# Kernel optimization log

Measured on AMD Instinct MI355X. Metric: run time of the kernel, lower is better.

The kernel has to match this reference:

```python
import jax, jax.numpy as jnp
import numpy as np

G = 128        # number of graphs
N = 512        # nodes per graph
F_IN = 128     # n_feat
H = 128        # agg_hidden
L = 5          # n_layer
FC = 128       # fc_hidden
C = 10         # n_class
E_HALF = 8192  # undirected edge pairs per graph (symmetrized -> 16384 directed)


def setup_inputs() -> dict:
    key = jax.random.key(0)
    ks = jax.random.split(key, 8)
    x = jax.random.normal(ks[0], (G * N, F_IN), dtype=jnp.float32)
    # per-graph random edges, offset into the block-diagonal node index space
    s = jax.random.randint(ks[1], (G, E_HALF), 0, N)
    d = jax.random.randint(ks[2], (G, E_HALF), 0, N)
    off = (jnp.arange(G) * N)[:, None]
    s = (s + off).reshape(-1)
    d = (d + off).reshape(-1)
    src = jnp.concatenate([s, d])  # symmetric adjacency (edges + reversed)
    dst = jnp.concatenate([d, s])
    eps = jnp.zeros((L,), jnp.float32)  # nn.Parameter(torch.zeros(n_layer))
    W = jax.random.normal(ks[3], (L, H, H), jnp.float32) / jnp.sqrt(H)
    b = jnp.zeros((L, H), jnp.float32)
    fc1_w = jax.random.normal(ks[4], (H, FC), jnp.float32) / jnp.sqrt(H)
    fc1_b = jnp.zeros((FC,), jnp.float32)
    fc2_w = jax.random.normal(ks[5], (FC, C), jnp.float32) / jnp.sqrt(FC)
    fc2_b = jnp.zeros((C,), jnp.float32)
    return {"x": x, "eps": eps, "W": W, "b": b,
            "fc1_w": fc1_w, "fc1_b": fc1_b, "fc2_w": fc2_w, "fc2_b": fc2_b,
            "src": src, "dst": dst}


def reference(x, eps, W, b, fc1_w, fc1_b, fc2_w, fc2_b, src, dst):
    n = x.shape[0]
    h = x
    for i in range(L):
        # sparse Adj @ h : gather along src, scatter-add to dst
        pooled = jax.ops.segment_sum(h[src], dst, num_segments=n)
        h = jax.nn.relu(((1.0 + eps[i]) * h + pooled) @ W[i] + b[i])
        # dropout p=0.0 / eval mode -> identity
    hg = h.reshape(G, N, -1).sum(axis=1)          # sum readout over nodes
    hg = jax.nn.relu(hg @ fc1_w + fc1_b)
    return jax.nn.softmax(hg @ fc2_w + fc2_b, axis=-1)
```

## Files before the change

kernel.cpp:

```cpp
#include <hip/hip_runtime.h>

#define NODES 65536
#define GNUM  128
#define NPG   512
#define FDIM  128

#define OFF_A   0u
#define OFF_WT  (32u<<20)
#define OFF_HTA (33u<<20)
#define OFF_HTB (49u<<20)

typedef short bf16x8 __attribute__((ext_vector_type(8)));
typedef float f32x4  __attribute__((ext_vector_type(4)));
typedef unsigned short u16;

#define GLB_AS __attribute__((address_space(1)))
#define LDS_AS __attribute__((address_space(3)))

static __device__ inline void gload16(const void* g, void* l) {
    __builtin_amdgcn_global_load_lds((const GLB_AS unsigned*)g,
                                     (LDS_AS unsigned*)l, 16, 0, 0);
}

static __device__ inline unsigned bf1(float x) {
    unsigned b = __float_as_uint(x);
    return (b + 0x7fffu + ((b >> 16) & 1u)) >> 16;
}
static __device__ inline unsigned pack_bf2(float x, float y) {
    return bf1(x) | (bf1(y) << 16);
}
static __device__ inline bf16x8 cvt8(uint2 au) {
    union { bf16x8 v; unsigned u[4]; } r;
#pragma unroll
    for (int i = 0; i < 2; ++i) {
        unsigned x = i ? au.y : au.x;
        float f0 = (float)(x & 0xffu);
        float f1 = (float)((x >> 8) & 0xffu);
        float f2 = (float)((x >> 16) & 0xffu);
        float f3 = (float)(x >> 24);
        r.u[i * 2]     = (__float_as_uint(f0) >> 16) | (__float_as_uint(f1) & 0xffff0000u);
        r.u[i * 2 + 1] = (__float_as_uint(f2) >> 16) | (__float_as_uint(f3) & 0xffff0000u);
    }
    return r.v;
}

__global__ __launch_bounds__(256) void k_cvtT(const float* __restrict__ x,
                                              u16* __restrict__ hT) {
    __shared__ char Cs[128 * 144];
    int t = threadIdx.x;
    int m0 = blockIdx.x * 64;
    int g = m0 >> 9, ml0 = m0 & 511;
#pragma unroll
    for (int it = 0; it < 8; ++it) {
        int i = t + 256 * it;
        int nl = i >> 5, fq = i & 31;
        float4 v = *(const float4*)(x + (size_t)(m0 + nl) * FDIM + fq * 4);
        *(u16*)(Cs + (fq * 4 + 0) * 144 + nl * 2) = (u16)bf1(v.x);
        *(u16*)(Cs + (fq * 4 + 1) * 144 + nl * 2) = (u16)bf1(v.y);
        *(u16*)(Cs + (fq * 4 + 2) * 144 + nl * 2) = (u16)bf1(v.z);
        *(u16*)(Cs + (fq * 4 + 3) * 144 + nl * 2) = (u16)bf1(v.w);
    }
    __syncthreads();
    u16* hg = hT + (size_t)g * 65536 + ml0;
#pragma unroll
    for (int j = 0; j < 4; ++j) {
        int idx = t + 256 * j;
        int f = idx >> 3, piece = idx & 7;
        uint4 v = *(const uint4*)(Cs + f * 144 + piece * 16);
        *(uint4*)((char*)(hg + (size_t)f * 512) + piece * 16) = v;
    }
}

__global__ __launch_bounds__(256) void k_wt(const float* __restrict__ W,
                                            u16* __restrict__ wt) {
    int idx = blockIdx.x * 256 + threadIdx.x;
    int l = idx >> 14, r = idx & 16383;
    int n = r >> 7, k = r & 127;
    wt[idx] = (u16)bf1(W[(l << 14) + k * 128 + n]);
}

__global__ __launch_bounds__(512) void k_adense(const int* __restrict__ src,
                                                const int* __restrict__ dst,
                                                unsigned* __restrict__ A,
                                                int halfE) {
    __shared__ unsigned cnt[128 * 128];
    int g = blockIdx.x >> 2, dq = blockIdx.x & 3;
    int t = threadIdx.x;
    for (int i = t; i < 128 * 128; i += 512) cnt[i] = 0u;
    __syncthreads();
    int dlo = dq * 128;
    int epg = halfE / GNUM;
#pragma unroll
    for (int r = 0; r < 2; ++r) {
        int base = r * halfE + g * epg;
        const int4* s4 = (const int4*)(src + base);
        const int4* d4 = (const int4*)(dst + base);
        for (int i = t; i < epg / 4; i += 512) {
            int4 sv = s4[i], dv = d4[i];
            int s, dl;
            s = sv.x & (NPG - 1); dl = (dv.x & (NPG - 1)) - dlo;
            if ((unsigned)dl < 128u) atomicAdd(&cnt[dl * 128 + (s >> 2)], 1u << ((s & 3) * 8));
            s = sv.y & (NPG - 1); dl = (dv.y & (NPG - 1)) - dlo;
            if ((unsigned)dl < 128u) atomicAdd(&cnt[dl * 128 + (s >> 2)], 1u << ((s & 3) * 8));
            s = sv.z & (NPG - 1); dl = (dv.z & (NPG - 1)) - dlo;
            if ((unsigned)dl < 128u) atomicAdd(&cnt[dl * 128 + (s >> 2)], 1u << ((s & 3) * 8));
            s = sv.w & (NPG - 1); dl = (dv.w & (NPG - 1)) - dlo;
            if ((unsigned)dl < 128u) atomicAdd(&cnt[dl * 128 + (s >> 2)], 1u << ((s & 3) * 8));
        }
    }
    __syncthreads();
    uint4* Ao = (uint4*)(A + ((size_t)g * 512 + dlo) * 128);
    const uint4* ls = (const uint4*)cnt;
    for (int i = t; i < 128 * 32; i += 512) Ao[i] = ls[i];
}

__global__ __launch_bounds__(512, 4) void k_layer(const u16* __restrict__ hT,
                                                  u16* __restrict__ hTo,
                                                  const unsigned char* __restrict__ A,
                                                  const u16* __restrict__ wt,
                                                  const float* __restrict__ bias,
                                                  const float* __restrict__ eps) {
    __shared__ uint4 smem16[59392 / 16];
    char* smem = (char*)smem16;
    char* Ps = smem + 24576;
    int t = threadIdx.x;
    int w = t >> 6, lane = t & 63;
    int q = lane >> 4, ln = lane & 15;
    int g = blockIdx.x & 127, dq = blockIdx.x >> 7;
    const unsigned char* Ab = A + (size_t)g * (512 * 512) + (size_t)dq * 128 * 512;
    const u16* hb = hT + (size_t)g * 65536;

    int pA = w * 64 + lane;
    int rowA = pA >> 2;
    const unsigned char* gA = Ab + (size_t)rowA * 512 + (((pA & 3) ^ (rowA & 3)) << 4);
    char* lA = smem + pA * 16;
    int pB0 = w * 128 + lane, pB1 = pB0 + 64;
    int fB0 = pB0 >> 3, fB1 = pB1 >> 3;
    const char* gB0 = (const char*)hb + (size_t)fB0 * 1024 + (((pB0 & 7) ^ (fB0 & 7)) << 4);
    const char* gB1 = (const char*)hb + (size_t)fB1 * 1024 + (((pB1 & 7) ^ (fB1 & 7)) << 4);
    char* lB0 = smem + 8192 + pB0 * 16;
    char* lB1 = smem + 8192 + pB1 * 16;

    f32x4 acc[8];
#pragma unroll
    for (int nt = 0; nt < 8; ++nt) acc[nt] = (f32x4){0.f, 0.f, 0.f, 0.f};

    int rA = w * 16 + ln;
    for (int ch = 0; ch < 8; ++ch) {
        __syncthreads();
        gload16(gA + ch * 64, lA);
        gload16(gB0 + ch * 128, lB0);
        gload16(gB1 + ch * 128, lB1);
        __syncthreads();
#pragma unroll
        for (int kcL = 0; kcL < 2; ++kcL) {
            int sA = rA * 4 + ((kcL * 2 + (q >> 1)) ^ (rA & 3));
            bf16x8 af = cvt8(*(const uint2*)(smem + sA * 16 + (q & 1) * 8));
#pragma unroll
            for (int nt = 0; nt < 8; ++nt) {
                int f = nt * 16 + ln;
                int sB = f * 8 + ((kcL * 4 + q) ^ (f & 7));
                bf16x8 bf = *(const bf16x8*)(smem + 8192 + sB * 16);
                acc[nt] = __builtin_amdgcn_mfma_f32_16x16x32_bf16(af, bf, acc[nt], 0, 0, 0);
            }
        }
    }
    float ep = 1.f + eps[0];
    int rl0 = w * 16 + q * 4;
    int mb0 = dq * 128 + rl0;
#pragma unroll
    for (int nt = 0; nt < 8; ++nt) {
        int f = nt * 16 + ln;
        uint2 sv = *(const uint2*)(hb + (size_t)f * 512 + mb0);
        float s0 = __uint_as_float(sv.x << 16);
        float s1 = __uint_as_float(sv.x & 0xffff0000u);
        float s2 = __uint_as_float(sv.y << 16);
        float s3 = __uint_as_float(sv.y & 0xffff0000u);
        f32x4 a = acc[nt];
        *(u16*)(Ps + (rl0 + 0) * 272 + f * 2) = (u16)bf1(fmaf(ep, s0, a[0]));
        *(u16*)(Ps + (rl0 + 1) * 272 + f * 2) = (u16)bf1(fmaf(ep, s1, a[1]));
        *(u16*)(Ps + (rl0 + 2) * 272 + f * 2) = (u16)bf1(fmaf(ep, s2, a[2]));
        *(u16*)(Ps + (rl0 + 3) * 272 + f * 2) = (u16)bf1(fmaf(ep, s3, a[3]));
    }
    __syncthreads();
    f32x4 acc2[8];
#pragma unroll
    for (int nt = 0; nt < 8; ++nt) acc2[nt] = (f32x4){0.f, 0.f, 0.f, 0.f};
#pragma unroll
    for (int ks = 0; ks < 4; ++ks) {
        bf16x8 af = *(const bf16x8*)(Ps + rA * 272 + ks * 64 + q * 16);
#pragma unroll
        for (int nt = 0; nt < 8; ++nt) {
            bf16x8 bf = *(const bf16x8*)(wt + (size_t)(nt * 16 + ln) * 128 + ks * 32 + q * 8);
            acc2[nt] = __builtin_amdgcn_mfma_f32_16x16x32_bf16(af, bf, acc2[nt], 0, 0, 0);
        }
    }
    __syncthreads();
#pragma unroll
    for (int nt = 0; nt < 8; ++nt) {
        int n = nt * 16 + ln;
        float bv = bias[n];
        f32x4 a = acc2[nt];
        *(uint2*)(Ps + n * 272 + rl0 * 2) =
            make_uint2(pack_bf2(fmaxf(a[0] + bv, 0.f), fmaxf(a[1] + bv, 0.f)),
                       pack_bf2(fmaxf(a[2] + bv, 0.f), fmaxf(a[3] + bv, 0.f)));
    }
    __syncthreads();
    u16* ho = hTo + (size_t)g * 65536 + dq * 128;
#pragma unroll
    for (int j = 0; j < 4; ++j) {
        int idx = t + 512 * j;
        int f = idx >> 4, piece = idx & 15;
        uint4 v = *(const uint4*)(Ps + f * 272 + piece * 16);
        *(uint4*)((char*)(ho + (size_t)f * 512) + piece * 16) = v;
    }
}

__global__ __launch_bounds__(128) void k_r(const u16* __restrict__ hT,
                                           const float* __restrict__ fc1w,
                                           const float* __restrict__ fc1b,
                                           const float* __restrict__ fc2w,
                                           const float* __restrict__ fc2b,
                                           float* __restrict__ out) {
    __shared__ float hg[128], z[128], lg[10];
    int g = blockIdx.x, t = threadIdx.x;
    const uint4* row = (const uint4*)(hT + (size_t)g * 65536 + (size_t)t * 512);
    float acc = 0.f;
#pragma unroll 4
    for (int i = 0; i < 64; ++i) {
        uint4 u = row[i];
        acc += __uint_as_float(u.x << 16) + __uint_as_float(u.x & 0xffff0000u);
        acc += __uint_as_float(u.y << 16) + __uint_as_float(u.y & 0xffff0000u);
        acc += __uint_as_float(u.z << 16) + __uint_as_float(u.z & 0xffff0000u);
        acc += __uint_as_float(u.w << 16) + __uint_as_float(u.w & 0xffff0000u);
    }
    hg[t] = acc;
    __syncthreads();
    float a1 = fc1b[t];
#pragma unroll 4
    for (int k = 0; k < 128; ++k) a1 = fmaf(hg[k], fc1w[k * 128 + t], a1);
    z[t] = fmaxf(a1, 0.f);
    __syncthreads();
    if (t < 10) {
        float l2 = fc2b[t];
        for (int k = 0; k < 128; ++k) l2 = fmaf(z[k], fc2w[k * 10 + t], l2);
        lg[t] = l2;
    }
    __syncthreads();
    if (t < 10) {
        float m = lg[0];
        for (int c = 1; c < 10; ++c) m = fmaxf(m, lg[c]);
        float ssum = 0.f;
        for (int c = 0; c < 10; ++c) ssum += expf(lg[c] - m);
        out[g * 10 + t] = expf(lg[t] - m) / ssum;
    }
}

extern "C" void kernel_launch(void* const* d_in, const int* in_sizes, int n_in,
                              void* d_out, int out_size, void* d_ws, size_t ws_size,
                              hipStream_t stream) {
    const float* x    = (const float*)d_in[0];
    const float* eps  = (const float*)d_in[1];
    const float* W    = (const float*)d_in[2];
    const float* b    = (const float*)d_in[3];
    const float* fc1w = (const float*)d_in[4];
    const float* fc1b = (const float*)d_in[5];
    const float* fc2w = (const float*)d_in[6];
    const float* fc2b = (const float*)d_in[7];
    const int*   src  = (const int*)d_in[8];
    const int*   dst  = (const int*)d_in[9];
    int E = in_sizes[8];
    int halfE = E >> 1;

    char* ws  = (char*)d_ws;
    unsigned char* Abuf = (unsigned char*)(ws + OFF_A);
    u16*  wtb = (u16*)(ws + OFF_WT);
    u16*  hta = (u16*)(ws + OFF_HTA);
    u16*  htb = (u16*)(ws + OFF_HTB);
    float* out = (float*)d_out;

    k_cvtT<<<NODES / 64, 256, 0, stream>>>(x, hta);
    k_wt<<<5 * 128 * 128 / 256, 256, 0, stream>>>(W, wtb);
    k_adense<<<GNUM * 4, 512, 0, stream>>>(src, dst, (unsigned*)Abuf, halfE);

    u16* cur = hta;
    u16* nxt = htb;
    for (int l = 0; l < 5; ++l) {
        k_layer<<<GNUM * 4, 512, 0, stream>>>(cur, nxt, Abuf,
                                              wtb + l * 128 * 128, b + l * 128, eps + l);
        u16* tmp = cur; cur = nxt; nxt = tmp;
    }
    k_r<<<GNUM, 128, 0, stream>>>(cur, fc1w, fc1b, fc2w, fc2b, out);
}
```

Baseline: 301.7 us.

## Pack adjacency counts as 4-bit nibbles and double-buffer layer LDS loads

New measurement: 292.4 us. 3.1% less time.

```diff
diff --git a/kernel.cpp b/kernel.cpp
--- a/kernel.cpp
+++ b/kernel.cpp
@@ -6,9 +6,9 @@
 #define FDIM  128
 
 #define OFF_A   0u
-#define OFF_WT  (32u<<20)
-#define OFF_HTA (33u<<20)
-#define OFF_HTB (49u<<20)
+#define OFF_WT  (16u<<20)
+#define OFF_HTA (17u<<20)
+#define OFF_HTB (33u<<20)
 
 typedef short bf16x8 __attribute__((ext_vector_type(8)));
 typedef float f32x4  __attribute__((ext_vector_type(4)));
@@ -29,17 +29,13 @@
 static __device__ inline unsigned pack_bf2(float x, float y) {
     return bf1(x) | (bf1(y) << 16);
 }
-static __device__ inline bf16x8 cvt8(uint2 au) {
+static __device__ inline bf16x8 cvt8n(unsigned x) {
     union { bf16x8 v; unsigned u[4]; } r;
 #pragma unroll
-    for (int i = 0; i < 2; ++i) {
-        unsigned x = i ? au.y : au.x;
-        float f0 = (float)(x & 0xffu);
-        float f1 = (float)((x >> 8) & 0xffu);
-        float f2 = (float)((x >> 16) & 0xffu);
-        float f3 = (float)(x >> 24);
-        r.u[i * 2]     = (__float_as_uint(f0) >> 16) | (__float_as_uint(f1) & 0xffff0000u);
-        r.u[i * 2 + 1] = (__float_as_uint(f2) >> 16) | (__float_as_uint(f3) & 0xffff0000u);
+    for (int i = 0; i < 4; ++i) {
+        float f0 = (float)((x >> (8 * i)) & 0xFu);
+        float f1 = (float)((x >> (8 * i + 4)) & 0xFu);
+        r.u[i] = (__float_as_uint(f0) >> 16) | (__float_as_uint(f1) & 0xffff0000u);
     }
     return r.v;
 }
@@ -81,12 +77,12 @@
 
 __global__ __launch_bounds__(512) void k_adense(const int* __restrict__ src,
                                                 const int* __restrict__ dst,
-                                                unsigned* __restrict__ A,
+                                                unsigned* __restrict__ A4,
                                                 int halfE) {
-    __shared__ unsigned cnt[128 * 128];
+    __shared__ unsigned cnt[128 * 64];
     int g = blockIdx.x >> 2, dq = blockIdx.x & 3;
     int t = threadIdx.x;
-    for (int i = t; i < 128 * 128; i += 512) cnt[i] = 0u;
+    for (int i = t; i < 128 * 64; i += 512) cnt[i] = 0u;
     __syncthreads();
     int dlo = dq * 128;
     int epg = halfE / GNUM;
@@ -99,19 +95,19 @@
             int4 sv = s4[i], dv = d4[i];
             int s, dl;
             s = sv.x & (NPG - 1); dl = (dv.x & (NPG - 1)) - dlo;
-            if ((unsigned)dl < 128u) atomicAdd(&cnt[dl * 128 + (s >> 2)], 1u << ((s & 3) * 8));
+            if ((unsigned)dl < 128u) atomicAdd(&cnt[dl * 64 + (s >> 3)], 1u << ((s & 7) * 4));
             s = sv.y & (NPG - 1); dl = (dv.y & (NPG - 1)) - dlo;
-            if ((unsigned)dl < 128u) atomicAdd(&cnt[dl * 128 + (s >> 2)], 1u << ((s & 3) * 8));
+            if ((unsigned)dl < 128u) atomicAdd(&cnt[dl * 64 + (s >> 3)], 1u << ((s & 7) * 4));
             s = sv.z & (NPG - 1); dl = (dv.z & (NPG - 1)) - dlo;
-            if ((unsigned)dl < 128u) atomicAdd(&cnt[dl * 128 + (s >> 2)], 1u << ((s & 3) * 8));
+            if ((unsigned)dl < 128u) atomicAdd(&cnt[dl * 64 + (s >> 3)], 1u << ((s & 7) * 4));
             s = sv.w & (NPG - 1); dl = (dv.w & (NPG - 1)) - dlo;
-            if ((unsigned)dl < 128u) atomicAdd(&cnt[dl * 128 + (s >> 2)], 1u << ((s & 3) * 8));
-        }
-    }
-    __syncthreads();
-    uint4* Ao = (uint4*)(A + ((size_t)g * 512 + dlo) * 128);
+            if ((unsigned)dl < 128u) atomicAdd(&cnt[dl * 64 + (s >> 3)], 1u << ((s & 7) * 4));
+        }
+    }
+    __syncthreads();
+    uint4* Ao = (uint4*)(A4 + ((size_t)g * 512 + dlo) * 64);
     const uint4* ls = (const uint4*)cnt;
-    for (int i = t; i < 128 * 32; i += 512) Ao[i] = ls[i];
+    for (int i = t; i < 128 * 16; i += 512) Ao[i] = ls[i];
 }
 
 __global__ __launch_bounds__(512, 4) void k_layer(const u16* __restrict__ hT,
@@ -120,50 +116,56 @@
                                                   const u16* __restrict__ wt,
                                                   const float* __restrict__ bias,
                                                   const float* __restrict__ eps) {
-    __shared__ uint4 smem16[59392 / 16];
+    __shared__ uint4 smem16[75776 / 16];
     char* smem = (char*)smem16;
-    char* Ps = smem + 24576;
+    char* Ps = smem + 40960;
     int t = threadIdx.x;
     int w = t >> 6, lane = t & 63;
     int q = lane >> 4, ln = lane & 15;
     int g = blockIdx.x & 127, dq = blockIdx.x >> 7;
-    const unsigned char* Ab = A + (size_t)g * (512 * 512) + (size_t)dq * 128 * 512;
+    const unsigned char* Ab = A + (size_t)g * (512 * 256) + (size_t)dq * 128 * 256;
     const u16* hb = hT + (size_t)g * 65536;
 
     int pA = w * 64 + lane;
-    int rowA = pA >> 2;
-    const unsigned char* gA = Ab + (size_t)rowA * 512 + (((pA & 3) ^ (rowA & 3)) << 4);
-    char* lA = smem + pA * 16;
+    int rowA = pA >> 1;
+    const unsigned char* gA = Ab + rowA * 256 + (pA & 1) * 16;
     int pB0 = w * 128 + lane, pB1 = pB0 + 64;
     int fB0 = pB0 >> 3, fB1 = pB1 >> 3;
     const char* gB0 = (const char*)hb + (size_t)fB0 * 1024 + (((pB0 & 7) ^ (fB0 & 7)) << 4);
     const char* gB1 = (const char*)hb + (size_t)fB1 * 1024 + (((pB1 & 7) ^ (fB1 & 7)) << 4);
-    char* lB0 = smem + 8192 + pB0 * 16;
-    char* lB1 = smem + 8192 + pB1 * 16;
 
     f32x4 acc[8];
 #pragma unroll
     for (int nt = 0; nt < 8; ++nt) acc[nt] = (f32x4){0.f, 0.f, 0.f, 0.f};
 
     int rA = w * 16 + ln;
+    if (w < 4) gload16(gA, smem + pA * 16);
+    gload16(gB0, smem + 8192 + pB0 * 16);
+    gload16(gB1, smem + 8192 + pB1 * 16);
+    __syncthreads();
     for (int ch = 0; ch < 8; ++ch) {
-        __syncthreads();
-        gload16(gA + ch * 64, lA);
-        gload16(gB0 + ch * 128, lB0);
-        gload16(gB1 + ch * 128, lB1);
-        __syncthreads();
+        char* Asc = smem + (ch & 1) * 4096;
+        char* Bsc = smem + 8192 + (ch & 1) * 16384;
+        if (ch < 7) {
+            char* Asn = smem + ((ch + 1) & 1) * 4096;
+            char* Bsn = smem + 8192 + ((ch + 1) & 1) * 16384;
+            if (w < 4) gload16(gA + (ch + 1) * 32, Asn + pA * 16);
+            gload16(gB0 + (ch + 1) * 128, Bsn + pB0 * 16);
+            gload16(gB1 + (ch + 1) * 128, Bsn + pB1 * 16);
+        }
 #pragma unroll
         for (int kcL = 0; kcL < 2; ++kcL) {
-            int sA = rA * 4 + ((kcL * 2 + (q >> 1)) ^ (rA & 3));
-            bf16x8 af = cvt8(*(const uint2*)(smem + sA * 16 + (q & 1) * 8));
+            unsigned a4 = *(const unsigned*)(Asc + rA * 32 + kcL * 16 + q * 4);
+            bf16x8 af = cvt8n(a4);
 #pragma unroll
             for (int nt = 0; nt < 8; ++nt) {
                 int f = nt * 16 + ln;
                 int sB = f * 8 + ((kcL * 4 + q) ^ (f & 7));
-                bf16x8 bf = *(const bf16x8*)(smem + 8192 + sB * 16);
+                bf16x8 bf = *(const bf16x8*)(Bsc + sB * 16);
                 acc[nt] = __builtin_amdgcn_mfma_f32_16x16x32_bf16(af, bf, acc[nt], 0, 0, 0);
             }
         }
+        __syncthreads();
     }
     float ep = 1.f + eps[0];
     int rl0 = w * 16 + q * 4;
```
